# Kernel tuning notes

Hardware: AMD Instinct MI355X
Metric: run time of the kernel (lower is better)

Reference implementation:

```python
import jax, jax.numpy as jnp
import numpy as np

N_NODES = 50000
N_EDGES = 800000
IN_C, HID_C, OUT_C = 256, 128, 64


def setup_inputs() -> dict:
    key = jax.random.key(0)
    k1, k2, k3, k4 = jax.random.split(key, 4)
    x = jax.random.normal(k1, (N_NODES, IN_C), dtype=jnp.float32)
    edge_index = jax.random.randint(k2, (2, N_EDGES), 0, N_NODES, dtype=jnp.int64)
    # Glorot-ish init for GCNConv weights; zero bias (PyG default)
    W1 = jax.random.normal(k3, (IN_C, HID_C), dtype=jnp.float32) * (1.0 / np.sqrt(IN_C))
    b1 = jnp.zeros((HID_C,), dtype=jnp.float32)
    W2 = jax.random.normal(k4, (HID_C, OUT_C), dtype=jnp.float32) * (1.0 / np.sqrt(HID_C))
    b2 = jnpform = jnp.zeros((OUT_C,), dtype=jnp.float32)
    return {"x": x, "edge_index": edge_index, "W1": W1, "b1": b1, "W2": W2, "b2": b2}


def _gcn_conv(x, src, dst, W, b, n_nodes):
    """PyG GCNConv: out = D^-1/2 (A+I) D^-1/2 x W + b (self-loops already in src/dst)."""
    h = x @ W  # [N, out] dense GEMM first (in >= out)
    deg = jax.ops.segment_sum(jnp.ones_like(dst, dtype=h.dtype), dst,
                              num_segments=n_nodes)  # includes self-loops -> deg >= 1
    dinv = jax.lax.rsqrt(jnp.maximum(deg, 1.0))
    norm = dinv[src] * dinv[dst]  # [E+N]
    msg = h[src] * norm[:, None]  # gather + scale
    out = jax.ops.segment_sum(msg, dst, num_segments=n_nodes)  # scatter-add
    return out + b


def reference(x, edge_index, W1, b1, W2, b2):
    n = x.shape[0]
    loops = jnp.arange(n, dtype=edge_index.dtype)
    src = jnp.concatenate([edge_index[0], loops])
    dst = jnp.concatenate([edge_index[1], loops])
    h = jax.nn.relu(_gcn_conv(x, src, dst, W1, b1, n))
    return _gcn_conv(h, src, dst, W2, b2, n)
```

## Files before the change

### kernel.cpp

```cpp
#include <hip/hip_runtime.h>

#define N_NODES 50000
#define N_EDGES 800000
#define IN_C    256
#define HID_C   128
#define OUT_C   64

#define SCAN_CHUNK 512
#define SCAN_NB ((N_NODES + SCAN_CHUNK - 1) / SCAN_CHUNK)

#define NBK 391
#define PCH 2048
#define NPB ((N_EDGES + PCH - 1) / PCH)

typedef __attribute__((ext_vector_type(8))) __bf16 bf16x8;
typedef __attribute__((ext_vector_type(4))) float f32x4;

__device__ __forceinline__ unsigned short f2bf(float f) {
    union { float f; unsigned int u; } c{f};
    unsigned int r = c.u + 0x7FFFu + ((c.u >> 16) & 1u);
    return (unsigned short)(r >> 16);
}
__device__ __forceinline__ float bf2f(unsigned short b) {
    union { unsigned int u; float f; } c{(unsigned int)b << 16};
    return c.f;
}

__global__ void deg_kernel(const int* __restrict__ src,
                           const int* __restrict__ dst,
                           unsigned int* __restrict__ deg, int E) {
    int i = blockIdx.x * blockDim.x + threadIdx.x;
    if (i < E) {
        int s = src[i];
        int d = dst[i];
        if ((unsigned)s < N_NODES && (unsigned)d < N_NODES)
            atomicAdd(&deg[d], 1u);
    }
}

__global__ __launch_bounds__(256) void scan1_kernel(
        unsigned int* __restrict__ cur, unsigned int* __restrict__ bsum,
        float* __restrict__ dinv, int N) {
    __shared__ unsigned int lds[256];
    const int b = blockIdx.x;
    const int t = threadIdx.x;
    const int i0 = b * SCAN_CHUNK + 2 * t;

    unsigned e0 = (i0     < N) ? cur[i0]     : 0u;
    unsigned e1 = (i0 + 1 < N) ? cur[i0 + 1] : 0u;
    if (i0     < N) dinv[i0]     = rsqrtf((float)(e0 + 1u));
    if (i0 + 1 < N) dinv[i0 + 1] = rsqrtf((float)(e1 + 1u));

    unsigned p = e0 + e1;
    lds[t] = p;
    __syncthreads();
    for (int off = 1; off < 256; off <<= 1) {
        unsigned v = (t >= off) ? lds[t - off] : 0u;
        __syncthreads();
        lds[t] += v;
        __syncthreads();
    }
    unsigned excl = lds[t] - p;
    if (t == 255) bsum[b] = lds[255];
    if (i0     < N) cur[i0]     = excl;
    if (i0 + 1 < N) cur[i0 + 1] = excl + e0;
}

__global__ __launch_bounds__(256) void scan2_kernel(
        unsigned int* __restrict__ cur, const unsigned int* __restrict__ bsum,
        int N) {
    __shared__ unsigned int lds[256];
    const int b = blockIdx.x;
    const int t = threadIdx.x;
    lds[t] = (t < b && t < SCAN_NB) ? bsum[t] : 0u;
    __syncthreads();
    for (int off = 128; off > 0; off >>= 1) {
        if (t < off) lds[t] += lds[t + off];
        __syncthreads();
    }
    const unsigned offset = lds[0];
    const int i0 = b * SCAN_CHUNK + 2 * t;
    if (i0     < N) cur[i0]     += offset;
    if (i0 + 1 < N) cur[i0 + 1] += offset;
}

__global__ void binit_kernel(const unsigned int* __restrict__ cur,
                             unsigned int* __restrict__ bcur,
                             unsigned int* __restrict__ bbase) {
    int t = threadIdx.x;
    if (t < NBK) {
        unsigned v = cur[t * 128];
        bcur[t]  = v;
        bbase[t] = v;
    }
    if (t == NBK) bbase[NBK] = N_EDGES;
}

template <int KDIM, int NDIM>
__global__ __launch_bounds__(256) void fused_gemm_part_kernel(
        const float* __restrict__ A, const float* __restrict__ Bw,
        const float* __restrict__ dinv,
        unsigned short* __restrict__ Cout, int M,
        const int* __restrict__ src, const int* __restrict__ dst,
        unsigned int* __restrict__ bcur,
        unsigned long long* __restrict__ gpairs, int E) {
    __shared__ union {
        struct { unsigned short A[64][40]; unsigned short B[NDIM][40]; } g;
        struct { unsigned long long pairs[PCH];
                 unsigned int counts[512];
                 unsigned int starts[513];
                 unsigned int gbase[NBK];
                 unsigned int temp[256]; } p;
    } sh;

    const int bid  = blockIdx.x;
    const int t    = threadIdx.x;
    const int role = bid % 3;
    const int pb   = bid / 3;

    if (role == 2) {
        const int base = pb * PCH;
        for (int i = t; i < 512; i += 256) sh.p.counts[i] = 0;
        __syncthreads();

        int sreg[PCH / 256], dreg[PCH / 256];
        unsigned rreg[PCH / 256];
        bool val[PCH / 256];
#pragma unroll
        for (int j = 0; j < PCH / 256; ++j) {
            int i = base + j * 256 + t;
            val[j] = false;
            if (i < E) {
                int s = src[i], d = dst[i];
                if ((unsigned)s < N_NODES && (unsigned)d < N_NODES) {
                    val[j] = true; sreg[j] = s; dreg[j] = d;
                    rreg[j] = atomicAdd(&sh.p.counts[(unsigned)d >> 7], 1u);
                }
            }
        }
        __syncthreads();
        unsigned e0 = sh.p.counts[2 * t], e1 = sh.p.counts[2 * t + 1];
        unsigned pp = e0 + e1;
        sh.p.temp[t] = pp;
        __syncthreads();
        for (int off = 1; off < 256; off <<= 1) {
            unsigned v = (t >= off) ? sh.p.temp[t - off] : 0u;
            __syncthreads();
            sh.p.temp[t] += v;
            __syncthreads();
        }
        unsigned excl = sh.p.temp[t] - pp;
        sh.p.starts[2 * t]     = excl;
        sh.p.starts[2 * t + 1] = excl + e0;
        if (t == 255) sh.p.starts[512] = sh.p.temp[255];
        __syncthreads();
        for (int b = t; b < NBK; b += 256) {
            unsigned c = sh.p.counts[b];
            if (c) sh.p.gbase[b] = atomicAdd(&bcur[b], c);
        }
        __syncthreads();
#pragma unroll
        for (int j = 0; j < PCH / 256; ++j)
            if (val[j]) {
                unsigned b    = (unsigned)dreg[j] >> 7;
                unsigned slot = sh.p.starts[b] + rreg[j];
                sh.p.pairs[slot] =
                    ((unsigned long long)(unsigned)dreg[j] << 32) |
                    (unsigned)sreg[j];
            }
        __syncthreads();
        unsigned total = sh.p.starts[512];
        for (unsigned i = t; i < total; i += 256) {
            unsigned long long pd = sh.p.pairs[i];
            unsigned b    = (unsigned)(pd >> 32) >> 7;
            unsigned rank = i - sh.p.starts[b];
            gpairs[sh.p.gbase[b] + rank] = pd;
        }
        return;
    }

    const int gb = pb * 2 + role;
    if (gb >= (M + 63) / 64) return;
    constexpr int NF = NDIM / 16;
    const int block_row = gb * 64;
    const int w    = t >> 6;
    const int lane = t & 63;
    const int arow = lane & 15;
    const int g    = lane >> 4;

    f32x4 acc[NF] = {};

    for (int k0 = 0; k0 < KDIM; k0 += 32) {
#pragma unroll
        for (int q = 0; q < 2; ++q) {
            int u   = t * 2 + q;
            int row = u >> 3;
            int kq  = u & 7;
            int grow = block_row + row;
            if (grow >= M) grow = M - 1;
            float4 v = *(const float4*)&A[(size_t)grow * KDIM + k0 + kq * 4];
            ushort4 bb = {f2bf(v.x), f2bf(v.y), f2bf(v.z), f2bf(v.w)};
            *(ushort4*)&sh.g.A[row][kq * 4] = bb;
        }
#pragma unroll
        for (int q = 0; q < NDIM / 32; ++q) {
            int u    = t * (NDIM / 32) + q;
            int krow = u / (NDIM / 4);
            int c4   = u % (NDIM / 4);
            float4 v = *(const float4*)&Bw[(size_t)(k0 + krow) * NDIM + c4 * 4];
            sh.g.B[c4 * 4 + 0][krow] = f2bf(v.x);
            sh.g.B[c4 * 4 + 1][krow] = f2bf(v.y);
            sh.g.B[c4 * 4 + 2][krow] = f2bf(v.z);
            sh.g.B[c4 * 4 + 3][krow] = f2bf(v.w);
        }
        __syncthreads();

        bf16x8 af = *(const bf16x8*)&sh.g.A[w * 16 + arow][g * 8];
#pragma unroll
        for (int f = 0; f < NF; ++f) {
            bf16x8 bf_ = *(const bf16x8*)&sh.g.B[f * 16 + arow][g * 8];
            acc[f] = __builtin_amdgcn_mfma_f32_16x16x32_bf16(af, bf_, acc[f],
                                                             0, 0, 0);
        }
        __syncthreads();
    }

#pragma unroll
    for (int i = 0; i < 4; ++i) {
        int row = block_row + w * 16 + g * 4 + i;
        if (row < M) {
            float dv = dinv[row];
#pragma unroll
            for (int f = 0; f < NF; ++f)
                Cout[(size_t)row * NDIM + f * 16 + arow] = f2bf(dv * acc[f][i]);
        }
    }
}

__global__ __launch_bounds__(256) void fine_fill_kernel(
        const unsigned long long* __restrict__ gpairs,
        const unsigned int* __restrict__ bbase,
        unsigned int* __restrict__ cur,
        int* __restrict__ esrc, int N) {
    __shared__ unsigned int cnt[128];
    __shared__ unsigned int inc[128];
    const int b  = blockIdx.x;
    const int t  = threadIdx.x;
    const unsigned e0 = bbase[b], e1 = bbase[b + 1];
    const int node0 = b << 7;
    const int nn = min(128, N - node0);

    if (t < 128) cnt[t] = 0;
    __syncthreads();
    for (unsigned i = e0 + t; i < e1; i += 256) {
        unsigned d = (unsigned)(gpairs[i] >> 32);
        atomicAdd(&cnt[d - node0], 1u);
    }
    __syncthreads();
    if (t < 128) inc[t] = cnt[t];
    __syncthreads();
    for (int off = 1; off < 128; off <<= 1) {
        unsigned a = (t >= off && t < 128) ? inc[t - off] : 0u;
        __syncthreads();
        if (t < 128) inc[t] += a;
        __syncthreads();
    }
    if (t < 128) cnt[t] = inc[t] - cnt[t];
    __syncthreads();
    for (unsigned i = e0 + t; i < e1; i += 256) {
        unsigned long long pd = gpairs[i];
        unsigned d = (unsigned)(pd >> 32);
        unsigned r = atomicAdd(&cnt[d - node0], 1u);
        esrc[e0 + r] = (int)(unsigned)pd;
    }
    __syncthreads();
    if (t < nn) cur[node0 + t] = e0 + inc[t];
}

template <int KDIM, int NDIM>
__global__ __launch_bounds__(256) void mfma_gemm_kernel(
        const float* __restrict__ A, const float* __restrict__ Bw,
        const float* __restrict__ dinv,
        unsigned short* __restrict__ Cout, int M) {
    __shared__ unsigned short Alds[64][40];
    __shared__ unsigned short Blds[NDIM][40];

    const int t = threadIdx.x;
    constexpr int NF = NDIM / 16;
    const int block_row = blockIdx.x * 64;
    const int w    = t >> 6;
    const int lane = t & 63;
    const int arow = lane & 15;
    const int g    = lane >> 4;

    f32x4 acc[NF] = {};

    for (int k0 = 0; k0 < KDIM; k0 += 32) {
#pragma unroll
        for (int q = 0; q < 2; ++q) {
            int u   = t * 2 + q;
            int row = u >> 3;
            int kq  = u & 7;
            int grow = block_row + row;
            if (grow >= M) grow = M - 1;
            float4 v = *(const float4*)&A[(size_t)grow * KDIM + k0 + kq * 4];
            ushort4 bb = {f2bf(v.x), f2bf(v.y), f2bf(v.z), f2bf(v.w)};
            *(ushort4*)&Alds[row][kq * 4] = bb;
        }
#pragma unroll
        for (int q = 0; q < NDIM / 32; ++q) {
            int u    = t * (NDIM / 32) + q;
            int krow = u / (NDIM / 4);
            int c4   = u % (NDIM / 4);
            float4 v = *(const float4*)&Bw[(size_t)(k0 + krow) * NDIM + c4 * 4];
            Blds[c4 * 4 + 0][krow] = f2bf(v.x);
            Blds[c4 * 4 + 1][krow] = f2bf(v.y);
            Blds[c4 * 4 + 2][krow] = f2bf(v.z);
            Blds[c4 * 4 + 3][krow] = f2bf(v.w);
        }
        __syncthreads();

        bf16x8 af = *(const bf16x8*)&Alds[w * 16 + arow][g * 8];
#pragma unroll
        for (int f = 0; f < NF; ++f) {
            bf16x8 bf_ = *(const bf16x8*)&Blds[f * 16 + arow][g * 8];
            acc[f] = __builtin_amdgcn_mfma_f32_16x16x32_bf16(af, bf_, acc[f],
                                                             0, 0, 0);
        }
        __syncthreads();
    }

#pragma unroll
    for (int i = 0; i < 4; ++i) {
        int row = block_row + w * 16 + g * 4 + i;
        if (row < M) {
            float dv = dinv[row];
#pragma unroll
            for (int f = 0; f < NF; ++f)
                Cout[(size_t)row * NDIM + f * 16 + arow] = f2bf(dv * acc[f][i]);
        }
    }
}

template <int C, bool RELU>
__global__ __launch_bounds__(256) void gather_kernel(
        const unsigned int* __restrict__ cur,
        const int* __restrict__ esrc,
        const float* __restrict__ dinv,
        const unsigned short* __restrict__ h,
        const float* __restrict__ bias,
        float* __restrict__ out, int N) {
    constexpr int G = C / 4;
    int tid  = blockIdx.x * blockDim.x + threadIdx.x;
    int v    = tid / G;
    int lane = tid % G;
    if (v >= N) return;
    unsigned int start = (v == 0) ? 0u : cur[v - 1];
    unsigned int end   = cur[v];

    ushort4 hs = *(const ushort4*)&h[(size_t)v * C + lane * 4];
    float4 a0 = {bf2f(hs.x), bf2f(hs.y), bf2f(hs.z), bf2f(hs.w)};
    float4 a1 = {0.f, 0.f, 0.f, 0.f};
    float4 a2 = {0.f, 0.f, 0.f, 0.f};
    float4 a3 = {0.f, 0.f, 0.f, 0.f};

    unsigned int e = start;
    for (; e + 4 <= end; e += 4) {
        int s0 = esrc[e + 0];
        int s1 = esrc[e + 1];
        int s2 = esrc[e + 2];
        int s3 = esrc[e + 3];
        ushort4 v0 = *(const ushort4*)&h[(size_t)s0 * C + lane * 4];
        ushort4 v1 = *(const ushort4*)&h[(size_t)s1 * C + lane * 4];
        ushort4 v2 = *(const ushort4*)&h[(size_t)s2 * C + lane * 4];
        ushort4 v3 = *(const ushort4*)&h[(size_t)s3 * C + lane * 4];
        a0.x += bf2f(v0.x); a0.y += bf2f(v0.y); a0.z += bf2f(v0.z); a0.w += bf2f(v0.w);
        a1.x += bf2f(v1.x); a1.y += bf2f(v1.y); a1.z += bf2f(v1.z); a1.w += bf2f(v1.w);
        a2.x += bf2f(v2.x); a2.y += bf2f(v2.y); a2.z += bf2f(v2.z); a2.w += bf2f(v2.w);
        a3.x += bf2f(v3.x); a3.y += bf2f(v3.y); a3.z += bf2f(v3.z); a3.w += bf2f(v3.w);
    }
    for (; e < end; ++e) {
        int s = esrc[e];
        ushort4 v0 = *(const ushort4*)&h[(size_t)s * C + lane * 4];
        a0.x += bf2f(v0.x); a0.y += bf2f(v0.y); a0.z += bf2f(v0.z); a0.w += bf2f(v0.w);
    }
    float4 acc;
    acc.x = (a0.x + a1.x) + (a2.x + a3.x);
    acc.y = (a0.y + a1.y) + (a2.y + a3.y);
    acc.z = (a0.z + a1.z) + (a2.z + a3.z);
    acc.w = (a0.w + a1.w) + (a2.w + a3.w);

    float dv = dinv[v];
    float4 b = *(const float4*)&bias[lane * 4];
    float4 r;
    r.x = fmaf(dv, acc.x, b.x);
    r.y = fmaf(dv, acc.y, b.y);
    r.z = fmaf(dv, acc.z, b.z);
    r.w = fmaf(dv, acc.w, b.w);
    if (RELU) {
        r.x = fmaxf(r.x, 0.f);
        r.y = fmaxf(r.y, 0.f);
        r.z = fmaxf(r.z, 0.f);
        r.w = fmaxf(r.w, 0.f);
    }
    *(float4*)&out[(size_t)v * C + lane * 4] = r;
}

template <int C, int C4>
__global__ void scatter_kernel(const int* __restrict__ src,
                               const int* __restrict__ dst,
                               const float* __restrict__ dinv,
                               const float* __restrict__ h,
                               float* __restrict__ out, int E) {
    int tid  = blockIdx.x * blockDim.x + threadIdx.x;
    int e    = tid / C4;
    int lane = tid % C4;
    if (e >= E) return;
    int s = src[e];
    int d = dst[e];
    if ((unsigned)s >= N_NODES || (unsigned)d >= N_NODES) return;
    float norm = dinv[s] * dinv[d];
    float4 v = *(const float4*)&h[(size_t)s * C + lane * 4];
    float* o = &out[(size_t)d * C + lane * 4];
    unsafeAtomicAdd(o + 0, v.x * norm);
    unsafeAtomicAdd(o + 1, v.y * norm);
    unsafeAtomicAdd(o + 2, v.z * norm);
    unsafeAtomicAdd(o + 3, v.w * norm);
}

__global__ void dinv_only_kernel(const unsigned int* __restrict__ deg,
                                 float* __restrict__ dinv, int N) {
    int i = blockIdx.x * blockDim.x + threadIdx.x;
    if (i < N) dinv[i] = rsqrtf((float)(deg[i] + 1u));
}

template <int BM, int BN, int BK, int TM, int TN, int KDIM, int NDIM, bool BF16OUT>
__global__ __launch_bounds__(256) void gemm_kernel(
        const float* __restrict__ A, const float* __restrict__ B,
        void* __restrict__ Cout, int M) {
    __shared__ float As[BK][BM + 1];
    __shared__ float Bs[BK][BN];

    constexpr int TX = BN / TN;
    const int t  = threadIdx.x;
    const int tx = t % TX;
    const int ty = t / TX;
    const int block_row = blockIdx.x * BM;
    const int col_base  = blockIdx.y * BN;

    float acc[TM][TN] = {};

    for (int k0 = 0; k0 < KDIM; k0 += BK) {
        for (int i = t; i < BM * BK / 4; i += 256) {
            int row = i / (BK / 4);
            int c4  = i % (BK / 4);
            int grow = block_row + row;
            if (grow >= M) grow = M - 1;
            float4 v = *(const float4*)&A[(size_t)grow * KDIM + k0 + c4 * 4];
            As[c4 * 4 + 0][row] = v.x;
            As[c4 * 4 + 1][row] = v.y;
            As[c4 * 4 + 2][row] = v.z;
            As[c4 * 4 + 3][row] = v.w;
        }
        for (int i = t; i < BK * BN / 4; i += 256) {
            int row = i / (BN / 4);
            int c4  = i % (BN / 4);
            *(float4*)&Bs[row][c4 * 4] =
                *(const float4*)&B[(size_t)(k0 + row) * NDIM + col_base + c4 * 4];
        }
        __syncthreads();

#pragma unroll
        for (int kk = 0; kk < BK; ++kk) {
            float4 av = *(const float4*)&As[kk][ty * TM];
            float a_[4] = {av.x, av.y, av.z, av.w};
            float4 bv[TN / 4];
#pragma unroll
            for (int j4 = 0; j4 < TN / 4; ++j4)
                bv[j4] = *(const float4*)&Bs[kk][tx * 4 + j4 * (BN / 2)];
#pragma unroll
            for (int i = 0; i < TM; ++i) {
                float ai = a_[i];
#pragma unroll
                for (int j4 = 0; j4 < TN / 4; ++j4) {
                    acc[i][j4 * 4 + 0] = fmaf(ai, bv[j4].x, acc[i][j4 * 4 + 0]);
                    acc[i][j4 * 4 + 1] = fmaf(ai, bv[j4].y, acc[i][j4 * 4 + 1]);
                    acc[i][j4 * 4 + 2] = fmaf(ai, bv[j4].z, acc[i][j4 * 4 + 2]);
                    acc[i][j4 * 4 + 3] = fmaf(ai, bv[j4].w, acc[i][j4 * 4 + 3]);
                }
            }
        }
        __syncthreads();
    }

#pragma unroll
    for (int i = 0; i < TM; ++i) {
        int grow = block_row + ty * TM + i;
        if (grow < M) {
#pragma unroll
            for (int j4 = 0; j4 < TN / 4; ++j4) {
                size_t idx = (size_t)grow * NDIM + col_base + tx * 4 + j4 * (BN / 2);
                if (BF16OUT) {
                    ushort4 w = {f2bf(acc[i][j4 * 4 + 0]), f2bf(acc[i][j4 * 4 + 1]),
                                 f2bf(acc[i][j4 * 4 + 2]), f2bf(acc[i][j4 * 4 + 3])};
                    *(ushort4*)&((unsigned short*)Cout)[idx] = w;
                } else {
                    float4 v = {acc[i][j4 * 4 + 0], acc[i][j4 * 4 + 1],
                                acc[i][j4 * 4 + 2], acc[i][j4 * 4 + 3]};
                    *(float4*)&((float*)Cout)[idx] = v;
                }
            }
        }
    }
}

template <int C, bool RELU>
__global__ void epilogue_kernel(const float* __restrict__ agg,
                                const float* __restrict__ h,
                                const float* __restrict__ dinv,
                                const float* __restrict__ bias,
                                float* __restrict__ out, int N) {
    int tid = blockIdx.x * blockDim.x + threadIdx.x;
    int total = N * (C / 4);
    if (tid >= total) return;
    int c4  = tid % (C / 4);
    int row = tid / (C / 4);
    float d2 = dinv[row];
    d2 *= d2;
    float4 a  = *(const float4*)&agg[(size_t)tid * 4];
    float4 hv = *(const float4*)&h[(size_t)tid * 4];
    float4 b  = *(const float4*)&bias[c4 * 4];
    float4 r;
    r.x = a.x + hv.x * d2 + b.x;
    r.y = a.y + hv.y * d2 + b.y;
    r.z = a.z + hv.z * d2 + b.z;
    r.w = a.w + hv.w * d2 + b.w;
    if (RELU) {
        r.x = fmaxf(r.x, 0.f);
        r.y = fmaxf(r.y, 0.f);
        r.z = fmaxf(r.z, 0.f);
        r.w = fmaxf(r.w, 0.f);
    }
    *(float4*)&out[(size_t)tid * 4] = r;
}

extern "C" void kernel_launch(void* const* d_in, const int* in_sizes, int n_in,
                              void* d_out, int out_size, void* d_ws, size_t ws_size,
                              hipStream_t stream) {
    const float* x   = (const float*)d_in[0];
    const int*   ei  = (const int*)d_in[1];
    const float* W1  = (const float*)d_in[2];
    const float* b1  = (const float*)d_in[3];
    const float* W2  = (const float*)d_in[4];
    const float* b2  = (const float*)d_in[5];
    float*       out = (float*)d_out;

    const int* src = ei;
    const int* dst = ei + N_EDGES;

    char* ws = (char*)d_ws;
    size_t off = 0;
    auto alloc = [&](size_t bytes) {
        void* p = ws + off;
        off += (bytes + 255) & ~(size_t)255;
        return p;
    };

    unsigned int*       cur    = (unsigned int*)alloc(N_NODES * sizeof(unsigned int));
    unsigned int*       bsum   = (unsigned int*)alloc(SCAN_NB * sizeof(unsigned int));
    float*              dinv   = (float*)alloc(N_NODES * sizeof(float));
    int*                esrc   = (int*)alloc((size_t)N_EDGES * sizeof(int));
    unsigned long long* gpairs = (unsigned long long*)alloc((size_t)N_EDGES * 8);
    unsigned int*       bbase  = (unsigned int*)alloc((NBK + 1) * sizeof(unsigned int));
    unsigned int*       bcur   = (unsigned int*)alloc(NBK * sizeof(unsigned int));
    unsigned short*     h1     = (unsigned short*)alloc((size_t)N_NODES * HID_C * 2);
    float*              g1     = (float*)alloc((size_t)N_NODES * HID_C * sizeof(float));
    unsigned short*     h2     = h1;
    size_t needed = off;

    if (ws_size >= needed) {
        hipMemsetAsync(cur, 0, N_NODES * sizeof(unsigned int), stream);

        deg_kernel<<<(N_EDGES + 255) / 256, 256, 0, stream>>>(src, dst, cur,
                                                              N_EDGES);
        scan1_kernel<<<SCAN_NB, 256, 0, stream>>>(cur, bsum, dinv, N_NODES);
        scan2_kernel<<<SCAN_NB, 256, 0, stream>>>(cur, bsum, N_NODES);
        binit_kernel<<<1, 512, 0, stream>>>(cur, bcur, bbase);

        fused_gemm_part_kernel<IN_C, HID_C>
            <<<3 * NPB, 256, 0, stream>>>(x, W1, dinv, h1, N_NODES,
                                          src, dst, bcur, gpairs, N_EDGES);
        fine_fill_kernel<<<NBK, 256, 0, stream>>>(gpairs, bbase, cur, esrc,
                                                  N_NODES);
        {
            int total = N_NODES * (HID_C / 4);
            gather_kernel<HID_C, true>
                <<<(total + 255) / 256, 256, 0, stream>>>(cur, esrc, dinv, h1,
                                                          b1, g1, N_NODES);
        }
        mfma_gemm_kernel<HID_C, OUT_C>
            <<<(N_NODES + 63) / 64, 256, 0, stream>>>(g1, W2, dinv, h2, N_NODES);
        {
            int total = N_NODES * (OUT_C / 4);
            gather_kernel<OUT_C, false>
                <<<(total + 255) / 256, 256, 0, stream>>>(cur, esrc, dinv, h2,
                                                          b2, out, N_NODES);
        }
    } else {
        off = 0;
        unsigned int* deg   = (unsigned int*)alloc(N_NODES * sizeof(unsigned int));
        float*        dinvF = (float*)alloc(N_NODES * sizeof(float));
        float*        h1F   = (float*)alloc((size_t)N_NODES * HID_C * sizeof(float));
        float*        agg1  = (float*)alloc((size_t)N_NODES * HID_C * sizeof(float));
        float*        h2F   = h1F;

        hipMemsetAsync(deg, 0, N_NODES * sizeof(unsigned int), stream);
        hipMemsetAsync(agg1, 0, (size_t)N_NODES * HID_C * sizeof(float), stream);
        hipMemsetAsync(out, 0, (size_t)N_NODES * OUT_C * sizeof(float), stream);

        deg_kernel<<<(N_EDGES + 255) / 256, 256, 0, stream>>>(src, dst, deg,
                                                              N_EDGES);
        dinv_only_kernel<<<(N_NODES + 255) / 256, 256, 0, stream>>>(deg, dinvF,
                                                                    N_NODES);

        gemm_kernel<64, 64, 16, 4, 4, IN_C, HID_C, false>
            <<<dim3((N_NODES + 63) / 64, HID_C / 64), 256, 0, stream>>>(
                x, W1, h1F, N_NODES);
        {
            long long total = (long long)N_EDGES * (HID_C / 4);
            scatter_kernel<HID_C, HID_C / 4>
                <<<(unsigned)((total + 255) / 256), 256, 0, stream>>>(
                    src, dst, dinvF, h1F, agg1, N_EDGES);
        }
        {
            int total = N_NODES * (HID_C / 4);
            epilogue_kernel<HID_C, true>
                <<<(total + 255) / 256, 256, 0, stream>>>(agg1, h1F, dinvF, b1,
                                                          agg1, N_NODES);
        }
        gemm_kernel<64, 64, 16, 4, 4, HID_C, OUT_C, false>
            <<<dim3((N_NODES + 63) / 64, OUT_C / 64), 256, 0, stream>>>(
                agg1, W2, h2F, N_NODES);
        {
            long long total = (long long)N_EDGES * (OUT_C / 4);
            scatter_kernel<OUT_C, OUT_C / 4>
                <<<(unsigned)((total + 255) / 256), 256, 0, stream>>>(
                    src, dst, dinvF, h2F, out, N_EDGES);
        }
        {
            int total = N_NODES * (OUT_C / 4);
            epilogue_kernel<OUT_C, false>
                <<<(total + 255) / 256, 256, 0, stream>>>(out, h2F, dinvF, b2,
                                                          out, N_NODES);
        }
    }
}
```

Before: 158.3 us.

## Pre-transpose weights to bf16, pack edge pairs to 32 bits, store g1 as bf16

The deg kernel now also converts W1 and W2 once into transposed bf16 copies, so the GEMM kernels load B tiles with 16-byte copies instead of a strided fp32 load, convert and transpose on every k-step. Edge partition pairs are packed into 32 bits (bucket, local dst, src) instead of 64, halving the scratch traffic between partitioning and the fine fill. The layer-1 gather writes bf16 output, and the second GEMM reads it directly, cutting intermediate bandwidth. The 16-bit src field assumes node ids below 65536, which holds for 50000 nodes but would silently break for larger graphs.

```diff
diff --git a/kernel.cpp b/kernel.cpp
--- a/kernel.cpp
+++ b/kernel.cpp
@@ -28,8 +28,33 @@
 
 __global__ void deg_kernel(const int* __restrict__ src,
                            const int* __restrict__ dst,
-                           unsigned int* __restrict__ deg, int E) {
-    int i = blockIdx.x * blockDim.x + threadIdx.x;
+                           unsigned int* __restrict__ deg, int E,
+                           const float* __restrict__ W1,
+                           const float* __restrict__ W2,
+                           unsigned short* __restrict__ Wt1,
+                           unsigned short* __restrict__ Wt2) {
+    const int bid = blockIdx.x;
+    const int t   = threadIdx.x;
+    if (Wt1 != nullptr && bid < 40) {
+        if (bid < 32) {
+            int e = bid * 1024 + t * 4;
+            float4 v = *(const float4*)&W1[e];
+            int k = e >> 7, c = e & 127;
+            Wt1[(c + 0) * IN_C + k] = f2bf(v.x);
+            Wt1[(c + 1) * IN_C + k] = f2bf(v.y);
+            Wt1[(c + 2) * IN_C + k] = f2bf(v.z);
+            Wt1[(c + 3) * IN_C + k] = f2bf(v.w);
+        } else {
+            int e = (bid - 32) * 1024 + t * 4;
+            float4 v = *(const float4*)&W2[e];
+            int k = e >> 6, c = e & 63;
+            Wt2[(c + 0) * HID_C + k] = f2bf(v.x);
+            Wt2[(c + 1) * HID_C + k] = f2bf(v.y);
+            Wt2[(c + 2) * HID_C + k] = f2bf(v.z);
+            Wt2[(c + 3) * HID_C + k] = f2bf(v.w);
+        }
+    }
+    int i = bid * blockDim.x + t;
     if (i < E) {
         int s = src[i];
         int d = dst[i];
@@ -98,15 +123,15 @@
 
 template <int KDIM, int NDIM>
 __global__ __launch_bounds__(256) void fused_gemm_part_kernel(
-        const float* __restrict__ A, const float* __restrict__ Bw,
+        const float* __restrict__ A, const unsigned short* __restrict__ Wt,
         const float* __restrict__ dinv,
         unsigned short* __restrict__ Cout, int M,
         const int* __restrict__ src, const int* __restrict__ dst,
         unsigned int* __restrict__ bcur,
-        unsigned long long* __restrict__ gpairs, int E) {
+        unsigned int* __restrict__ gpairs, int E) {
     __shared__ union {
         struct { unsigned short A[64][40]; unsigned short B[NDIM][40]; } g;
-        struct { unsigned long long pairs[PCH];
+        struct { unsigned int pairs[PCH];
                  unsigned int counts[512];
                  unsigned int starts[513];
                  unsigned int gbase[NBK];
@@ -123,8 +148,7 @@
         for (int i = t; i < 512; i += 256) sh.p.counts[i] = 0;
         __syncthreads();
 
-        int sreg[PCH / 256], dreg[PCH / 256];
-        unsigned rreg[PCH / 256];
+        unsigned preg[PCH / 256], rreg[PCH / 256];
         bool val[PCH / 256];
 #pragma unroll
         for (int j = 0; j < PCH / 256; ++j) {
@@ -133,8 +157,11 @@
             if (i < E) {
                 int s = src[i], d = dst[i];
                 if ((unsigned)s < N_NODES && (unsigned)d < N_NODES) {
-                    val[j] = true; sreg[j] = s; dreg[j] = d;
-                    rreg[j] = atomicAdd(&sh.p.counts[(unsigned)d >> 7], 1u);
+                    val[j] = true;
+                    unsigned bkt = (unsigned)d >> 7;
+                    preg[j] = (bkt << 23) | (((unsigned)d & 127u) << 16) |
+                              (unsigned)s;
+                    rreg[j] = atomicAdd(&sh.p.counts[bkt], 1u);
                 }
             }
         }
@@ -162,19 +189,17 @@
 #pragma unroll
         for (int j = 0; j < PCH / 256; ++j)
             if (val[j]) {
-                unsigned b    = (unsigned)dreg[j] >> 7;
-                unsigned slot = sh.p.starts[b] + rreg[j];
-                sh.p.pairs[slot] =
-                    ((unsigned long long)(unsigned)dreg[j] << 32) |
-                    (unsigned)sreg[j];
+                unsigned bkt  = preg[j] >> 23;
+                unsigned slot = sh.p.starts[bkt] + rreg[j];
+                sh.p.pairs[slot] = preg[j];
             }
         __syncthreads();
         unsigned total = sh.p.starts[512];
         for (unsigned i = t; i < total; i += 256) {
-            unsigned long long pd = sh.p.pairs[i];
-            unsigned b    = (unsigned)(pd >> 32) >> 7;
-            unsigned rank = i - sh.p.starts[b];
-            gpairs[sh.p.gbase[b] + rank] = pd;
+            unsigned pd  = sh.p.pairs[i];
+            unsigned bkt = pd >> 23;
+            unsigned rank = i - sh.p.starts[bkt];
+            gpairs[sh.p.gbase[bkt] + rank] = pd;
         }
         return;
     }
@@ -202,16 +227,16 @@
             ushort4 bb = {f2bf(v.x), f2bf(v.y), f2bf(v.z), f2bf(v.w)};
             *(ushort4*)&sh.g.A[row][kq * 4] = bb;
         }
-#pragma unroll
-        for (int q = 0; q < NDIM / 32; ++q) {
-            int u    = t * (NDIM / 32) + q;
-            int krow = u / (NDIM / 4);
-            int c4   = u % (NDIM / 4);
-            float4 v = *(const float4*)&Bw[(size_t)(k0 + krow) * NDIM + c4 * 4];
-            sh.g.B[c4 * 4 + 0][krow] = f2bf(v.x);
-            sh.g.B[c4 * 4 + 1][krow] = f2bf(v.y);
-            sh.g.B[c4 * 4 + 2][krow] = f2bf(v.z);
-            sh.g.B[c4 * 4 + 3][krow] = f2bf(v.w);
+        {
+            constexpr int B8 = (NDIM * 4) / 256;
+#pragma unroll
+            for (int r = 0; r < B8; ++r) {
+                int iu  = t * B8 + r;
+                int col = iu >> 2;
+                int k8  = iu & 3;
+                *(uint4*)&sh.g.B[col][k8 * 8] =
+                    *(const uint4*)&Wt[(size_t)col * KDIM + k0 + k8 * 8];
+            }
         }
         __syncthreads();
 
@@ -238,7 +263,7 @@
 }
 
 __global__ __launch_bounds__(256) void fine_fill_kernel(
-        const unsigned long long* __restrict__ gpairs,
+        const unsigned int* __restrict__ gpairs,
         const unsigned int* __restrict__ bbase,
         unsigned int* __restrict__ cur,
         int* __restrict__ esrc, int N) {
@@ -253,8 +278,8 @@
     if (t < 128) cnt[t] = 0;
     __syncthreads();
     for (unsigned i = e0 + t; i < e1; i += 256) {
-        unsigned d = (unsigned)(gpairs[i] >> 32);
-        atomicAdd(&cnt[d - node0], 1u);
+        unsigned dloc = (gpairs[i] >> 16) & 127u;
+        atomicAdd(&cnt[dloc], 1u);
     }
     __syncthreads();
     if (t < 128) inc[t] = cnt[t];
@@ -268,18 +293,18 @@
     if (t < 128) cnt[t] = inc[t] - cnt[t];
     __syncthreads();
     for (unsigned i = e0 + t; i < e1; i += 256) {
-        unsigned long long pd = gpairs[i];
-        unsigned d = (unsigned)(pd >> 32);
-        unsigned r = atomicAdd(&cnt[d - node0], 1u);
-        esrc[e0 + r] = (int)(unsigned)pd;
+        unsigned pd   = gpairs[i];
+        unsigned dloc = (pd >> 16) & 127u;
+        unsigned r = atomicAdd(&cnt[dloc], 1u);
+        esrc[e0 + r] = (int)(pd & 0xFFFFu);
     }
     __syncthreads();
     if (t < nn) cur[node0 + t] = e0 + inc[t];
 }
 
-template <int KDIM, int NDIM>
+template <int KDIM, int NDIM, bool ABF16>
 __global__ __launch_bounds__(256) void mfma_gemm_kernel(
-        const float* __restrict__ A, const float* __restrict__ Bw,
+        const void* __restrict__ Ain, const unsigned short* __restrict__ Wt,
         const float* __restrict__ dinv,
         unsigned short* __restrict__ Cout, int M) {
     __shared__ unsigned short Alds[64][40];
@@ -296,27 +321,38 @@
     f32x4 acc[NF] = {};
 
     for (int k0 = 0; k0 < KDIM; k0 += 32) {
-#pragma unroll
-        for (int q = 0; q < 2; ++q) {
-            int u   = t * 2 + q;
-            int row = u >> 3;
-            int kq  = u & 7;
+        if (ABF16) {
+            const unsigned short* A = (const unsigned short*)Ain;
+            int row = t >> 2;
+            int k8  = t & 3;
             int grow = block_row + row;
             if (grow >= M) grow = M - 1;
-            float4 v = *(const float4*)&A[(size_t)grow * KDIM + k0 + kq * 4];
-            ushort4 bb = {f2bf(v.x), f2bf(v.y), f2bf(v.z), f2bf(v.w)};
-            *(ushort4*)&Alds[row][kq * 4] = bb;
-        }
-#pragma unroll
-        for (int q = 0; q < NDIM / 32; ++q) {
-            int u    = t * (NDIM / 32) + q;
-            int krow = u / (NDIM / 4);
-            int c4   = u % (NDIM / 4);
-            float4 v = *(const float4*)&Bw[(size_t)(k0 + krow) * NDIM + c4 * 4];
-            Blds[c4 * 4 + 0][krow] = f2bf(v.x);
-            Blds[c4 * 4 + 1][krow] = f2bf(v.y);
-            Blds[c4 * 4 + 2][krow] = f2bf(v.z);
-            Blds[c4 * 4 + 3][krow] = f2bf(v.w);
+            *(uint4*)&Alds[row][k8 * 8] =
+                *(const uint4*)&A[(size_t)grow * KDIM + k0 + k8 * 8];
+        } else {
+            const float* A = (const float*)Ain;
+#pragma unroll
+            for (int q = 0; q < 2; ++q) {
+                int u   = t * 2 + q;
+                int row = u >> 3;
+                int kq  = u & 7;
+                int grow = block_row + row;
+                if (grow >= M) grow = M - 1;
+                float4 v = *(const float4*)&A[(size_t)grow * KDIM + k0 + kq * 4];
+                ushort4 bb = {f2bf(v.x), f2bf(v.y), f2bf(v.z), f2bf(v.w)};
+                *(ushort4*)&Alds[row][kq * 4] = bb;
+            }
+        }
+        {
+            constexpr int B8 = (NDIM * 4) / 256;
+#pragma unroll
+            for (int r = 0; r < B8; ++r) {
+                int iu  = t * B8 + r;
+                int col = iu >> 2;
+                int k8  = iu & 3;
+                *(uint4*)&Blds[col][k8 * 8] =
+                    *(const uint4*)&Wt[(size_t)col * KDIM + k0 + k8 * 8];
+            }
         }
         __syncthreads();
 
@@ -342,14 +378,14 @@
     }
 }
 
-template <int C, bool RELU>
+template <int C, bool RELU, bool OUTBF16>
 __global__ __launch_bounds__(256) void gather_kernel(
         const unsigned int* __restrict__ cur,
         const int* __restrict__ esrc,
         const float* __restrict__ dinv,
         const unsigned short* __restrict__ h,
         const float* __restrict__ bias,
-        float* __restrict__ out, int N) {
+        void* __restrict__ out, int N) {
     constexpr int G = C / 4;
     int tid  = blockIdx.x * blockDim.x + threadIdx.x;
     int v    = tid / G;
@@ -403,7 +439,12 @@
         r.z = fmaxf(r.z, 0.f);
         r.w = fmaxf(r.w, 0.f);
     }
-    *(float4*)&out[(size_t)v * C + lane * 4] = r;
+    if (OUTBF16) {
+        ushort4 o = {f2bf(r.x), f2bf(r.y), f2bf(r.z), f2bf(r.w)};
+        *(ushort4*)&((unsigned short*)out)[(size_t)v * C + lane * 4] = o;
+    } else {
+        *(float4*)&((float*)out)[(size_t)v * C + lane * 4] = r;
+    }
 }
 
 template <int C, int C4>
@@ -434,10 +475,10 @@
     if (i < N) dinv[i] = rsqrtf((float)(deg[i] + 1u));
 }
 
-template <int BM, int BN, int BK, int TM, int TN, int KDIM, int NDIM, bool BF16OUT>
+template <int BM, int BN, int BK, int TM, int TN, int KDIM, int NDIM>
 __global__ __launch_bounds__(256) void gemm_kernel(
         const float* __restrict__ A, const float* __restrict__ B,
-        void* __restrict__ Cout, int M) {
+        float* __restrict__ Cout, int M) {
     __shared__ float As[BK][BM + 1];
     __shared__ float Bs[BK][BN];
 
@@ -499,16 +540,10 @@
         if (grow < M) {
 #pragma unroll
             for (int j4 = 0; j4 < TN / 4; ++j4) {
-                size_t idx = (size_t)grow * NDIM + col_base + tx * 4 + j4 * (BN / 2);
-                if (BF16OUT) {
-                    ushort4 w = {f2bf(acc[i][j4 * 4 + 0]), f2bf(acc[i][j4 * 4 + 1]),
-                                 f2bf(acc[i][j4 * 4 + 2]), f2bf(acc[i][j4 * 4 + 3])};
-                    *(ushort4*)&((unsigned short*)Cout)[idx] = w;
-                } else {
-                    float4 v = {acc[i][j4 * 4 + 0], acc[i][j4 * 4 + 1],
-                                acc[i][j4 * 4 + 2], acc[i][j4 * 4 + 3]};
-                    *(float4*)&((float*)Cout)[idx] = v;
-                }
+                float4 v = {acc[i][j4 * 4 + 0], acc[i][j4 * 4 + 1],
+                            acc[i][j4 * 4 + 2], acc[i][j4 * 4 + 3]};
+                *(float4*)&Cout[(size_t)grow * NDIM + col_base + tx * 4 +
+                                j4 * (BN / 2)] = v;
             }
         }
     }
@@ -566,43 +601,46 @@
         return p;
     };
 
-    unsigned int*       cur    = (unsigned int*)alloc(N_NODES * sizeof(unsigned int));
-    unsigned int*       bsum   = (unsigned int*)alloc(SCAN_NB * sizeof(unsigned int));
-    float*              dinv   = (float*)alloc(N_NODES * sizeof(float));
-    int*                esrc   = (int*)alloc((size_t)N_EDGES * sizeof(int));
-    unsigned long long* gpairs = (unsigned long long*)alloc((size_t)N_EDGES * 8);
-    unsigned int*       bbase  = (unsigned int*)alloc((NBK + 1) * sizeof(unsigned int));
-    unsigned int*       bcur   = (unsigned int*)alloc(NBK * sizeof(unsigned int));
-    unsigned short*     h1     = (unsigned short*)alloc((size_t)N_NODES * HID_C * 2);
-    float*              g1     = (float*)alloc((size_t)N_NODES * HID_C * sizeof(float));
-    unsigned short*     h2     = h1;
+    unsigned int*   cur    = (unsigned int*)alloc(N_NODES * sizeof(unsigned int));
+    unsigned int*   bsum   = (unsigned int*)alloc(SCAN_NB * sizeof(unsigned int));
+    float*          dinv   = (float*)alloc(N_NODES * sizeof(float));
+    int*            esrc   = (int*)alloc((size_t)N_EDGES * sizeof(int));
+    unsigned int*   gpairs = (unsigned int*)alloc((size_t)N_EDGES * 4);
+    unsigned int*   bbase  = (unsigned int*)alloc((NBK + 1) * sizeof(unsigned int));
+    unsigned int*   bcur   = (unsigned int*)alloc(NBK * sizeof(unsigned int));
+    unsigned short* Wt1    = (unsigned short*)alloc((size_t)IN_C * HID_C * 2);
+    unsigned short* Wt2    = (unsigned short*)alloc((size_t)HID_C * OUT_C * 2);
+    unsigned short* h1     = (unsigned short*)alloc((size_t)N_NODES * HID_C * 2);
+    unsigned short* g1     = (unsigned short*)alloc((size_t)N_NODES * HID_C * 2);
+    unsigned short* h2     = h1;
     size_t needed = off;
 
     if (ws_size >= needed) {
         hipMemsetAsync(cur, 0, N_NODES * sizeof(unsigned int), stream);
 
-        deg_kernel<<<(N_EDGES + 255) / 256, 256, 0, stream>>>(src, dst, cur,
-                                                              N_EDGES);
+        deg_kernel<<<(N_EDGES + 255) / 256, 256, 0, stream>>>(
+            src, dst, cur, N_EDGES, W1, W2, Wt1, Wt2);
         scan1_kernel<<<SCAN_NB, 256, 0, stream>>>(cur, bsum, dinv, N_NODES);
         scan2_kernel<<<SCAN_NB, 256, 0, stream>>>(cur, bsum, N_NODES);
         binit_kernel<<<1, 512, 0, stream>>>(cur, bcur, bbase);
 
         fused_gemm_part_kernel<IN_C, HID_C>
-            <<<3 * NPB, 256, 0, stream>>>(x, W1, dinv, h1, N_NODES,
+            <<<3 * NPB, 256, 0, stream>>>(x, Wt1, dinv, h1, N_NODES,
                                           src, dst, bcur, gpairs, N_EDGES);
         fine_fill_kernel<<<NBK, 256, 0, stream>>>(gpairs, bbase, cur, esrc,
                                                   N_NODES);
         {
             int total = N_NODES * (HID_C / 4);
-            gather_kernel<HID_C, true>
+            gather_kernel<HID_C, true, true>
                 <<<(total + 255) / 256, 256, 0, stream>>>(cur, esrc, dinv, h1,
                                                           b1, g1, N_NODES);
         }
-        mfma_gemm_kernel<HID_C, OUT_C>
-            <<<(N_NODES + 63) / 64, 256, 0, stream>>>(g1, W2, dinv, h2, N_NODES);
+        mfma_gemm_kernel<HID_C, OUT_C, true>
+            <<<(N_NODES + 63) / 64, 256, 0, stream>>>(g1, Wt2, dinv, h2,
+                                                      N_NODES);
         {
             int total = N_NODES * (OUT_C / 4);
-            gather_kernel<OUT_C, false>
+            gather_kernel<OUT_C, false, false>
                 <<<(total + 255) / 256, 256, 0, stream>>>(cur, esrc, dinv, h2,
                                                           b2, out, N_NODES);
         }
@@ -618,12 +656,12 @@
         hipMemsetAsync(agg1, 0, (size_t)N_NODES * HID_C * sizeof(float), stream);
         hipMemsetAsync(out, 0, (size_t)N_NODES * OUT_C * sizeof(float), stream);
 
-        deg_kernel<<<(N_EDGES + 255) / 256, 256, 0, stream>>>(src, dst, deg,
-                                                              N_EDGES);
+        deg_kernel<<<(N_EDGES + 255) / 256, 256, 0, stream>>>(
+            src, dst, deg, N_EDGES, nullptr, nullptr, nullptr, nullptr);
         dinv_only_kernel<<<(N_NODES + 255) / 256, 256, 0, stream>>>(deg, dinvF,
                                                                     N_NODES);
 
-        gemm_kernel<64, 64, 16, 4, 4, IN_C, HID_C, false>
+        gemm_kernel<64, 64, 16, 4, 4, IN_C, HID_C>
             <<<dim3((N_NODES + 63) / 64, HID_C / 64), 256, 0, stream>>>(
                 x, W1, h1F, N_NODES);
         {
@@ -638,7 +676,7 @@
                 <<<(total + 255) / 256, 256, 0, stream>>>(agg1, h1F, dinvF, b1,
                                                           agg1, N_NODES);
         }
-        gemm_kernel<64, 64, 16, 4, 4, HID_C, OUT_C, false>
+        gemm_kernel<64, 64, 16, 4, 4, HID_C, OUT_C>
             <<<dim3((N_NODES + 63) / 64, OUT_C / 64), 256, 0, stream>>>(
                 agg1, W2, h2F, N_NODES);
         {
```

New measurement: 149.3 us. 5.7% less time.
